# Kernel optimization log

Hardware: AMD Instinct MI355X
Metric: run time of the kernel (lower is better)

## Reference

```python
import jax, jax.numpy as jnp
import numpy as np

N_NODES = 50000
N_EDGES = 800000
IN_DIM = 768
HIDDEN = 256
N_CLASSES = 10
N_GRAPHS = 128


def setup_inputs() -> dict:
    key = jax.random.key(0)
    ks = jax.random.split(key, 10)
    emb = jax.random.normal(ks[0], (N_NODES, IN_DIM), dtype=jnp.float32)
    edge_index = jax.random.randint(ks[1], (2, N_EDGES), 0, N_NODES, dtype=jnp.int32)
    batch = jnp.sort(jax.random.randint(ks[2], (N_NODES,), 0, N_GRAPHS, dtype=jnp.int32))
    # GCNConv weights (glorot-ish scale) and biases
    W1 = jax.random.normal(ks[3], (IN_DIM, HIDDEN), dtype=jnp.float32) / np.sqrt(IN_DIM)
    b1 = jnp.zeros((HIDDEN,), dtype=jnp.float32)
    W2 = jax.random.normal(ks[4], (HIDDEN, HIDDEN), dtype=jnp.float32) / np.sqrt(HIDDEN)
    b2 = jnp.zeros((HIDDEN,), dtype=jnp.float32)
    Wfc = jax.random.normal(ks[5], (HIDDEN, N_CLASSES), dtype=jnp.float32) / np.sqrt(HIDDEN)
    bfc = jnp.zeros((N_CLASSES,), dtype=jnp.float32)
    return {"emb": emb, "edge_index": edge_index, "batch": batch,
            "W1": W1, "b1": b1, "W2": W2, "b2": b2, "Wfc": Wfc, "bfc": bfc}


def _gcn_conv(x, src, dst, W, b, n_nodes):
    # PyG GCNConv: x' = D^{-1/2} (A + I) D^{-1/2} X W + b, self-loops included
    h = x @ W                                   # [N, H] dense GEMM
    deg = jax.ops.segment_sum(jnp.ones_like(dst, dtype=h.dtype), dst,
                              num_segments=n_nodes)
    dinv = jnp.where(deg > 0, jax.lax.rsqrt(deg), 0.0)
    norm = dinv[src] * dinv[dst]                # [E+N]
    msgs = h[src] * norm[:, None]               # gather [E+N, H]
    out = jax.ops.segment_sum(msgs, dst, num_segments=n_nodes)  # scatter-add
    return out + b


def reference(emb, edge_index, batch, W1, b1, W2, b2, Wfc, bfc):
    n_nodes = emb.shape[0]
    loops = jnp.arange(n_nodes, dtype=edge_index.dtype)
    src = jnp.concatenate([edge_index[0], loops])  # add self-loops
    dst = jnp.concatenate([edge_index[1], loops])

    x = jax.nn.relu(_gcn_conv(emb, src, dst, W1, b1, n_nodes))
    # F.dropout(p=0.3) is a no-op in eval mode (training=False)
    x = _gcn_conv(x, src, dst, W2, b2, n_nodes)

    # global_mean_pool over graph ids
    sums = jax.ops.segment_sum(x, batch, num_segments=N_GRAPHS)
    cnts = jax.ops.segment_sum(jnp.ones((n_nodes,), dtype=x.dtype), batch,
                               num_segments=N_GRAPHS)
    pooled = sums / jnp.maximum(cnts, 1.0)[:, None]  # [G, H]
    return pooled @ Wfc + bfc                        # [G, C]
```

## Files before the change

### kernel.cpp

```cpp
#include <hip/hip_runtime.h>

#define N_NODES 50000
#define N_EDGES 800000
#define IN_DIM 768
#define HIDDEN 256
#define N_CLASSES 10
#define N_GRAPHS 128

typedef __attribute__((ext_vector_type(8))) short bf16x8;
typedef __attribute__((ext_vector_type(4))) float f32x4;
typedef __attribute__((ext_vector_type(8))) unsigned short u16x8;

__device__ __forceinline__ float bf2f(unsigned short u) {
    union { unsigned int i; float f; } c; c.i = ((unsigned int)u) << 16; return c.f;
}
__device__ __forceinline__ unsigned short f2bf(float f) {
    unsigned int x = __float_as_uint(f);
    return (unsigned short)((x + 0x7fffu + ((x >> 16) & 1u)) >> 16);
}

__device__ __forceinline__ void gload16(const void* g, void* l) {
    __builtin_amdgcn_global_load_lds((const __attribute__((address_space(1))) void*)g,
                                     (__attribute__((address_space(3))) void*)l, 16, 0, 0);
}

__global__ void zero_int(int* p, int n) {
    int i = blockIdx.x * blockDim.x + threadIdx.x;
    if (i < n) p[i] = 0;
}

__global__ void zero_f32(float* p, int n) {
    int i = blockIdx.x * blockDim.x + threadIdx.x;
    if (i < n) p[i] = 0.f;
}

__global__ void hist_dst(const int* __restrict__ dst, int* __restrict__ cnt) {
    int e = blockIdx.x * blockDim.x + threadIdx.x;
    if (e < N_EDGES) atomicAdd(&cnt[dst[e]], 1);
}

__global__ __launch_bounds__(1024) void scan_kernel(const int* __restrict__ cnt,
                                                    int* __restrict__ rowstart,
                                                    int* __restrict__ cursor,
                                                    float* __restrict__ dinv) {
    __shared__ int wsum[16];
    __shared__ int chunk_carry;
    const int tid = threadIdx.x, lane = tid & 63, wid = tid >> 6;
    if (tid == 0) chunk_carry = 0;
    __syncthreads();
    for (int base = 0; base < N_NODES; base += 1024) {
        int i = base + tid;
        int v = (i < N_NODES) ? cnt[i] : 0;
        if (i < N_NODES) dinv[i] = rsqrtf(1.0f + (float)v);
        int s = v;
#pragma unroll
        for (int d = 1; d < 64; d <<= 1) { int t = __shfl_up(s, d); if (lane >= d) s += t; }
        if (lane == 63) wsum[wid] = s;
        __syncthreads();
        if (tid < 16) {
            int ww = wsum[tid];
#pragma unroll
            for (int d = 1; d < 16; d <<= 1) { int t = __shfl_up(ww, d); if (tid >= d) ww += t; }
            wsum[tid] = ww;
        }
        __syncthreads();
        int wpre = (wid == 0) ? 0 : wsum[wid - 1];
        int excl = chunk_carry + wpre + s - v;
        if (i < N_NODES) { rowstart[i] = excl; cursor[i] = excl; }
        int total = wsum[15];
        __syncthreads();
        if (tid == 0) chunk_carry += total;
        __syncthreads();
    }
    if (threadIdx.x == 0) rowstart[N_NODES] = chunk_carry;
}

__global__ void scatter_edges(const int* __restrict__ src, const int* __restrict__ dst,
                              int* __restrict__ cursor, int* __restrict__ col) {
    int e = blockIdx.x * blockDim.x + threadIdx.x;
    if (e >= N_EDGES) return;
    int d = dst[e];
    int pos = atomicAdd(&cursor[d], 1);
    col[pos] = src[e];
}

__global__ __launch_bounds__(256) void transpose_w_bf16(const float* __restrict__ W,
                                                        unsigned short* __restrict__ WT, int K) {
    __shared__ float t[32][33];
    int tx = threadIdx.x & 31, ty = threadIdx.x >> 5;
    int k0 = blockIdx.x * 32, n0 = blockIdx.y * 32;
#pragma unroll
    for (int i = 0; i < 4; ++i) {
        int k = k0 + ty + i * 8;
        t[ty + i * 8][tx] = W[(size_t)k * 256 + n0 + tx];
    }
    __syncthreads();
#pragma unroll
    for (int i = 0; i < 4; ++i) {
        int n = n0 + ty + i * 8;
        WT[(size_t)n * K + k0 + tx] = f2bf(t[tx][ty + i * 8]);
    }
}

template <int K, bool CVT>
__global__ __launch_bounds__(256, 4) void gemm_mfma(const void* __restrict__ Av,
                                                    const unsigned short* __restrict__ BT,
                                                    unsigned short* __restrict__ C, int M) {
    __shared__ uint4 sm[2560];
    uint4* As = sm;
    uint4* Bs = sm + 512;
    const int tid = threadIdx.x;
    const int lane = tid & 63, w = tid >> 6;
    const int lr = lane & 15, kg = lane >> 4;
    const int bm = blockIdx.x * 64;

    f32x4 acc[16] = {};

    for (int k0 = 0; k0 < K; k0 += 64) {
        if constexpr (CVT) {
            const float* Af = (const float*)Av;
#pragma unroll
            for (int i = 0; i < 2; ++i) {
                int glin = i * 256 + tid, r = glin >> 3, g = glin & 7;
                int gs = g ^ (r & 7);
                int rg = bm + r; rg = rg < M ? rg : M - 1;
                const float* p = &Af[(size_t)rg * K + k0 + gs * 8];
                float4 u = *(const float4*)p;
                float4 v = *(const float4*)(p + 4);
                u16x8 o;
                o[0] = f2bf(u.x); o[1] = f2bf(u.y); o[2] = f2bf(u.z); o[3] = f2bf(u.w);
                o[4] = f2bf(v.x); o[5] = f2bf(v.y); o[6] = f2bf(v.z); o[7] = f2bf(v.w);
                *(u16x8*)&As[r * 8 + g] = o;
            }
        } else {
            const unsigned short* Ab = (const unsigned short*)Av;
#pragma unroll
            for (int i = 0; i < 2; ++i) {
                int glin = w * 128 + i * 64 + lane;
                int r = glin >> 3, g = glin & 7;
                int gs = g ^ (r & 7);
                int rg = bm + r; rg = rg < M ? rg : M - 1;
                gload16(&Ab[(size_t)rg * K + k0 + gs * 8], &As[w * 128 + i * 64]);
            }
        }
#pragma unroll
        for (int i = 0; i < 8; ++i) {
            int glin = w * 512 + i * 64 + lane;
            int n = glin >> 3, g = glin & 7;
            int gs = g ^ (n & 7);
            gload16(&BT[(size_t)n * K + k0 + gs * 8], &Bs[w * 512 + i * 64]);
        }
        __syncthreads();

#pragma unroll
        for (int h = 0; h < 2; ++h) {
            int r0 = 16 * w + lr;
            bf16x8 a0 = *(const bf16x8*)&As[r0 * 8 + ((4 * h + kg) ^ (r0 & 7))];
#pragma unroll
            for (int f = 0; f < 16; ++f) {
                int nr = 16 * f + lr;
                bf16x8 bf = *(const bf16x8*)&Bs[nr * 8 + ((4 * h + kg) ^ (nr & 7))];
                acc[f] = __builtin_amdgcn_mfma_f32_16x16x32_bf16(bf, a0, acc[f], 0, 0, 0);
            }
        }
        __syncthreads();
    }
    int orow = bm + 16 * w + lr;
    if (orow < M) {
#pragma unroll
        for (int f = 0; f < 16; ++f) {
            ushort4 o = make_ushort4(f2bf(acc[f][0]), f2bf(acc[f][1]),
                                     f2bf(acc[f][2]), f2bf(acc[f][3]));
            *(ushort4*)&C[(size_t)orow * 256 + 16 * f + 4 * kg] = o;
        }
    }
}

template <bool RELU, bool OUTBF>
__global__ __launch_bounds__(256) void agg_csr(const unsigned short* __restrict__ h,
                                               const float* __restrict__ dinv,
                                               const int* __restrict__ rowstart,
                                               const int* __restrict__ col,
                                               const float* __restrict__ bias,
                                               void* __restrict__ outv) {
    int node = (blockIdx.x * 256 + threadIdx.x) >> 6;
    if (node >= N_NODES) return;
    const int lane = threadIdx.x & 63;
    const int half = lane >> 5, sl = lane & 31;

    float dd = dinv[node];
    float acc[8] = {};

    {
        u16x8 hv = *(const u16x8*)&h[(size_t)node * 256 + sl * 8];
        float wgt = half ? 0.f : dd * dd;
#pragma unroll
        for (int i = 0; i < 8; ++i) acc[i] += bf2f(hv[i]) * wgt;
    }

    int j0 = rowstart[node], jend = rowstart[node + 1];
    for (int j = j0; j < jend; j += 2) {
        int sidx = j + half;
        bool p = sidx < jend;
        int s = p ? col[sidx] : node;
        float nrm = p ? dinv[s] * dd : 0.f;
        u16x8 v = *(const u16x8*)&h[(size_t)s * 256 + sl * 8];
#pragma unroll
        for (int i = 0; i < 8; ++i) acc[i] += bf2f(v[i]) * nrm;
    }

#pragma unroll
    for (int i = 0; i < 8; ++i) acc[i] += __shfl_xor(acc[i], 32);

    if (half == 0) {
        float4 b0 = *(const float4*)&bias[sl * 8];
        float4 b1 = *(const float4*)&bias[sl * 8 + 4];
        acc[0] += b0.x; acc[1] += b0.y; acc[2] += b0.z; acc[3] += b0.w;
        acc[4] += b1.x; acc[5] += b1.y; acc[6] += b1.z; acc[7] += b1.w;
        if (RELU) {
#pragma unroll
            for (int i = 0; i < 8; ++i) acc[i] = fmaxf(acc[i], 0.f);
        }
        if (OUTBF) {
            u16x8 o;
#pragma unroll
            for (int i = 0; i < 8; ++i) o[i] = f2bf(acc[i]);
            *(u16x8*)((unsigned short*)outv + (size_t)node * 256 + sl * 8) = o;
        } else {
            float* ob = (float*)outv + (size_t)node * 256 + sl * 8;
            *(float4*)ob = make_float4(acc[0], acc[1], acc[2], acc[3]);
            *(float4*)(ob + 4) = make_float4(acc[4], acc[5], acc[6], acc[7]);
        }
    }
}

#define POOL_CHUNK 49
__global__ __launch_bounds__(256) void pool_partial(const float* __restrict__ x,
                                                    const int* __restrict__ batch,
                                                    float* __restrict__ gsum) {
    int lo = blockIdx.x * POOL_CHUNK;
    if (lo >= N_NODES) return;
    int hi = lo + POOL_CHUNK; if (hi > N_NODES) hi = N_NODES;
    int c = threadIdx.x;
    int g = batch[lo];
    float acc = 0.f;
    for (int n = lo; n < hi; ++n) {
        int gn = batch[n];
        if (gn != g) { atomicAdd(&gsum[g * 256 + c], acc); acc = 0.f; g = gn; }
        acc += x[(size_t)n * 256 + c];
    }
    atomicAdd(&gsum[g * 256 + c], acc);
}

__global__ __launch_bounds__(256) void fc_head(const float* __restrict__ gsum,
                                               const int* __restrict__ batch,
                                               const float* __restrict__ Wfc,
                                               const float* __restrict__ bfc,
                                               float* __restrict__ out) {
    int g = blockIdx.x;
    int c = threadIdx.x;
    int lo = 0, hi = N_NODES;
    while (lo < hi) { int m = (lo + hi) >> 1; if (batch[m] < g) lo = m + 1; else hi = m; }
    int lo2 = lo, hi2 = N_NODES;
    while (lo2 < hi2) { int m = (lo2 + hi2) >> 1; if (batch[m] < g + 1) lo2 = m + 1; else hi2 = m; }
    float inv = 1.0f / fmaxf((float)(lo2 - lo), 1.0f);
    __shared__ float pooled[256];
    pooled[c] = gsum[(size_t)g * 256 + c] * inv;
    __syncthreads();
    if (c < N_CLASSES) {
        float acc = bfc[c];
        for (int k = 0; k < 256; ++k) acc += pooled[k] * Wfc[k * N_CLASSES + c];
        out[g * N_CLASSES + c] = acc;
    }
}

extern "C" void kernel_launch(void* const* d_in, const int* in_sizes, int n_in,
                              void* d_out, int out_size, void* d_ws, size_t ws_size,
                              hipStream_t stream) {
    const float* emb  = (const float*)d_in[0];
    const int*   eidx = (const int*)d_in[1];
    const int*   batch= (const int*)d_in[2];
    const float* W1   = (const float*)d_in[3];
    const float* b1   = (const float*)d_in[4];
    const float* W2   = (const float*)d_in[5];
    const float* b2   = (const float*)d_in[6];
    const float* Wfc  = (const float*)d_in[7];
    const float* bfc  = (const float*)d_in[8];
    float* out = (float*)d_out;

    const int* src = eidx;
    const int* dst = eidx + N_EDGES;

    char* ws = (char*)d_ws;
    size_t off = 0;
    auto alloc = [&](size_t bytes) { void* p = ws + off; off += (bytes + 1023) & ~(size_t)1023; return p; };
    int*   rowcnt   = (int*)alloc(N_NODES * 4);
    int*   rowstart = (int*)alloc((N_NODES + 1) * 4);
    int*   cursor   = (int*)alloc(N_NODES * 4);
    int*   col      = (int*)alloc(N_EDGES * 4);
    float* dinv     = (float*)alloc(N_NODES * 4);
    float* gsum     = (float*)alloc((size_t)N_GRAPHS * 256 * 4);
    unsigned short* W1T = (unsigned short*)alloc((size_t)HIDDEN * IN_DIM * 2);
    unsigned short* W2T = (unsigned short*)alloc((size_t)HIDDEN * HIDDEN * 2);
    unsigned short* bufH = (unsigned short*)alloc((size_t)N_NODES * 256 * 2);
    unsigned short* x1 = (unsigned short*)alloc((size_t)N_NODES * 256 * 2);
    float* x2 = (float*)alloc((size_t)N_NODES * 256 * 4);

    const int NB = (N_NODES + 255) / 256;
    const int EBk = (N_EDGES + 255) / 256;
    const int AGG_B = (N_NODES * 64 + 255) / 256;
    dim3 gemm_grid((N_NODES + 63) / 64, 1);
    const int POOL_B = (N_NODES + POOL_CHUNK - 1) / POOL_CHUNK;

    zero_int<<<NB, 256, 0, stream>>>(rowcnt, N_NODES);
    hist_dst<<<EBk, 256, 0, stream>>>(dst, rowcnt);
    scan_kernel<<<1, 1024, 0, stream>>>(rowcnt, rowstart, cursor, dinv);
    scatter_edges<<<EBk, 256, 0, stream>>>(src, dst, cursor, col);
    zero_f32<<<(N_GRAPHS * 256 + 255) / 256, 256, 0, stream>>>(gsum, N_GRAPHS * 256);

    transpose_w_bf16<<<dim3(IN_DIM / 32, 8), 256, 0, stream>>>(W1, W1T, IN_DIM);
    transpose_w_bf16<<<dim3(HIDDEN / 32, 8), 256, 0, stream>>>(W2, W2T, HIDDEN);

    gemm_mfma<IN_DIM, true><<<gemm_grid, 256, 0, stream>>>(emb, W1T, bufH, N_NODES);
    agg_csr<true, true><<<AGG_B, 256, 0, stream>>>(bufH, dinv, rowstart, col, b1, x1);

    gemm_mfma<HIDDEN, false><<<gemm_grid, 256, 0, stream>>>(x1, W2T, bufH, N_NODES);
    agg_csr<false, false><<<AGG_B, 256, 0, stream>>>(bufH, dinv, rowstart, col, b2, x2);

    pool_partial<<<POOL_B, 256, 0, stream>>>(x2, batch, gsum);
    fc_head<<<N_GRAPHS, 256, 0, stream>>>(gsum, batch, Wfc, bfc, out);
}
```

Measured before the change: 418.5 us.

## Double-buffer GEMM shared tiles and unroll CSR aggregation gathers by four

After: 396.4 us. 1.06x faster.

```diff
diff --git a/kernel.cpp b/kernel.cpp
--- a/kernel.cpp
+++ b/kernel.cpp
@@ -103,68 +103,105 @@
 }
 
 template <int K, bool CVT>
-__global__ __launch_bounds__(256, 4) void gemm_mfma(const void* __restrict__ Av,
+__global__ __launch_bounds__(256, 2) void gemm_mfma(const void* __restrict__ Av,
                                                     const unsigned short* __restrict__ BT,
                                                     unsigned short* __restrict__ C, int M) {
-    __shared__ uint4 sm[2560];
+    constexpr int NS = K / 64;
+    __shared__ uint4 sm[5120];
     uint4* As = sm;
-    uint4* Bs = sm + 512;
+    uint4* Bs = sm + 1024;
     const int tid = threadIdx.x;
     const int lane = tid & 63, w = tid >> 6;
     const int lr = lane & 15, kg = lane >> 4;
     const int bm = blockIdx.x * 64;
 
+    const int ra = tid >> 2;
+    const int ca = (tid & 3) * 2;
+    int rga = bm + ra; rga = rga < M ? rga : M - 1;
+
     f32x4 acc[16] = {};
 
-    for (int k0 = 0; k0 < K; k0 += 64) {
+    {
         if constexpr (CVT) {
-            const float* Af = (const float*)Av;
-#pragma unroll
-            for (int i = 0; i < 2; ++i) {
-                int glin = i * 256 + tid, r = glin >> 3, g = glin & 7;
-                int gs = g ^ (r & 7);
-                int rg = bm + r; rg = rg < M ? rg : M - 1;
-                const float* p = &Af[(size_t)rg * K + k0 + gs * 8];
-                float4 u = *(const float4*)p;
-                float4 v = *(const float4*)(p + 4);
-                u16x8 o;
-                o[0] = f2bf(u.x); o[1] = f2bf(u.y); o[2] = f2bf(u.z); o[3] = f2bf(u.w);
-                o[4] = f2bf(v.x); o[5] = f2bf(v.y); o[6] = f2bf(v.z); o[7] = f2bf(v.w);
-                *(u16x8*)&As[r * 8 + g] = o;
-            }
+            const float* p = &((const float*)Av)[(size_t)rga * K + ca * 8];
+            float4 u0 = ((const float4*)p)[0], u1 = ((const float4*)p)[1];
+            float4 u2 = ((const float4*)p)[2], u3 = ((const float4*)p)[3];
+            u16x8 o0, o1;
+            o0[0] = f2bf(u0.x); o0[1] = f2bf(u0.y); o0[2] = f2bf(u0.z); o0[3] = f2bf(u0.w);
+            o0[4] = f2bf(u1.x); o0[5] = f2bf(u1.y); o0[6] = f2bf(u1.z); o0[7] = f2bf(u1.w);
+            o1[0] = f2bf(u2.x); o1[1] = f2bf(u2.y); o1[2] = f2bf(u2.z); o1[3] = f2bf(u2.w);
+            o1[4] = f2bf(u3.x); o1[5] = f2bf(u3.y); o1[6] = f2bf(u3.z); o1[7] = f2bf(u3.w);
+            *(u16x8*)&As[ra * 8 + (ca ^ (ra & 7))] = o0;
+            *(u16x8*)&As[ra * 8 + ((ca + 1) ^ (ra & 7))] = o1;
         } else {
             const unsigned short* Ab = (const unsigned short*)Av;
-#pragma unroll
-            for (int i = 0; i < 2; ++i) {
-                int glin = w * 128 + i * 64 + lane;
-                int r = glin >> 3, g = glin & 7;
-                int gs = g ^ (r & 7);
-                int rg = bm + r; rg = rg < M ? rg : M - 1;
-                gload16(&Ab[(size_t)rg * K + k0 + gs * 8], &As[w * 128 + i * 64]);
-            }
+            uint4 v0 = *(const uint4*)&Ab[(size_t)rga * K + ca * 8];
+            uint4 v1 = *(const uint4*)&Ab[(size_t)rga * K + ca * 8 + 8];
+            As[ra * 8 + (ca ^ (ra & 7))] = v0;
+            As[ra * 8 + ((ca + 1) ^ (ra & 7))] = v1;
         }
 #pragma unroll
         for (int i = 0; i < 8; ++i) {
             int glin = w * 512 + i * 64 + lane;
             int n = glin >> 3, g = glin & 7;
             int gs = g ^ (n & 7);
-            gload16(&BT[(size_t)n * K + k0 + gs * 8], &Bs[w * 512 + i * 64]);
-        }
-        __syncthreads();
-
+            gload16(&BT[(size_t)n * K + gs * 8], &Bs[w * 512 + i * 64]);
+        }
+    }
+    __syncthreads();
+
+    for (int k = 0; k < NS; ++k) {
+        const int cur = k & 1, nxt = cur ^ 1;
+        const int kk1 = (k + 1) * 64;
+        float4 u0, u1, u2, u3;
+        uint4 v0, v1;
+        if (k + 1 < NS) {
+#pragma unroll
+            for (int i = 0; i < 8; ++i) {
+                int glin = w * 512 + i * 64 + lane;
+                int n = glin >> 3, g = glin & 7;
+                int gs = g ^ (n & 7);
+                gload16(&BT[(size_t)n * K + kk1 + gs * 8], &Bs[nxt * 2048 + w * 512 + i * 64]);
+            }
+            if constexpr (CVT) {
+                const float* p = &((const float*)Av)[(size_t)rga * K + kk1 + ca * 8];
+                u0 = ((const float4*)p)[0]; u1 = ((const float4*)p)[1];
+                u2 = ((const float4*)p)[2]; u3 = ((const float4*)p)[3];
+            } else {
+                const unsigned short* Ab = (const unsigned short*)Av;
+                v0 = *(const uint4*)&Ab[(size_t)rga * K + kk1 + ca * 8];
+                v1 = *(const uint4*)&Ab[(size_t)rga * K + kk1 + ca * 8 + 8];
+            }
+        }
 #pragma unroll
         for (int h = 0; h < 2; ++h) {
             int r0 = 16 * w + lr;
-            bf16x8 a0 = *(const bf16x8*)&As[r0 * 8 + ((4 * h + kg) ^ (r0 & 7))];
+            int gc = 4 * h + kg;
+            bf16x8 a0 = *(const bf16x8*)&As[cur * 512 + r0 * 8 + (gc ^ (r0 & 7))];
 #pragma unroll
             for (int f = 0; f < 16; ++f) {
                 int nr = 16 * f + lr;
-                bf16x8 bf = *(const bf16x8*)&Bs[nr * 8 + ((4 * h + kg) ^ (nr & 7))];
+                bf16x8 bf = *(const bf16x8*)&Bs[cur * 2048 + nr * 8 + (gc ^ (nr & 7))];
                 acc[f] = __builtin_amdgcn_mfma_f32_16x16x32_bf16(bf, a0, acc[f], 0, 0, 0);
             }
         }
-        __syncthreads();
-    }
+        if (k + 1 < NS) {
+            if constexpr (CVT) {
+                u16x8 o0, o1;
+                o0[0] = f2bf(u0.x); o0[1] = f2bf(u0.y); o0[2] = f2bf(u0.z); o0[3] = f2bf(u0.w);
+                o0[4] = f2bf(u1.x); o0[5] = f2bf(u1.y); o0[6] = f2bf(u1.z); o0[7] = f2bf(u1.w);
+                o1[0] = f2bf(u2.x); o1[1] = f2bf(u2.y); o1[2] = f2bf(u2.z); o1[3] = f2bf(u2.w);
+                o1[4] = f2bf(u3.x); o1[5] = f2bf(u3.y); o1[6] = f2bf(u3.z); o1[7] = f2bf(u3.w);
+                *(u16x8*)&As[nxt * 512 + ra * 8 + (ca ^ (ra & 7))] = o0;
+                *(u16x8*)&As[nxt * 512 + ra * 8 + ((ca + 1) ^ (ra & 7))] = o1;
+            } else {
+                As[nxt * 512 + ra * 8 + (ca ^ (ra & 7))] = v0;
+                As[nxt * 512 + ra * 8 + ((ca + 1) ^ (ra & 7))] = v1;
+            }
+        }
+        __syncthreads();
+    }
+
     int orow = bm + 16 * w + lr;
     if (orow < M) {
 #pragma unroll
@@ -199,7 +236,23 @@
     }
 
     int j0 = rowstart[node], jend = rowstart[node + 1];
-    for (int j = j0; j < jend; j += 2) {
+    int j = j0;
+    for (; j + 8 <= jend; j += 8) {
+        int s0 = col[j + half];
+        int s1 = col[j + 2 + half];
+        int s2 = col[j + 4 + half];
+        int s3 = col[j + 6 + half];
+        float n0 = dinv[s0] * dd, n1 = dinv[s1] * dd;
+        float n2 = dinv[s2] * dd, n3 = dinv[s3] * dd;
+        u16x8 v0 = *(const u16x8*)&h[(size_t)s0 * 256 + sl * 8];
+        u16x8 v1 = *(const u16x8*)&h[(size_t)s1 * 256 + sl * 8];
+        u16x8 v2 = *(const u16x8*)&h[(size_t)s2 * 256 + sl * 8];
+        u16x8 v3 = *(const u16x8*)&h[(size_t)s3 * 256 + sl * 8];
+#pragma unroll
+        for (int i = 0; i < 8; ++i)
+            acc[i] += bf2f(v0[i]) * n0 + bf2f(v1[i]) * n1 + bf2f(v2[i]) * n2 + bf2f(v3[i]) * n3;
+    }
+    for (; j < jend; j += 2) {
         int sidx = j + half;
         bool p = sidx < jend;
         int s = p ? col[sidx] : node;
```
